# Kernel optimization log

Hardware: AMD Instinct MI355X
Metric: run time of the kernel (lower is better)

Reference implementation:

```python
import jax, jax.numpy as jnp
import numpy as np

BIG = 1e10  # penalty for cross-batch pairs in masked knn


def knn_interpolate(x, pos, pos_skip, batch, batch_skip, k):
    # squared pairwise distances [N_skip, N] via ||a||^2 + ||b||^2 - 2 a.b (avoids [Ns,N,3] temp)
    d2 = (jnp.sum(pos_skip**2, -1)[:, None]
          + jnp.sum(pos**2, -1)[None, :]
          - 2.0 * (pos_skip @ pos.T))
    d2 = jnp.maximum(d2, 0.0)
    # mask out neighbors from a different cloud in the batch
    d2 = d2 + jnp.where(batch_skip[:, None] != batch[None, :], BIG, 0.0)
    neg_d2k, idx = jax.lax.top_k(-d2, k)          # k smallest distances
    d2k = -neg_d2k                                # [N_skip, k]
    w = 1.0 / jnp.clip(d2k, 1e-16)                # inverse squared-distance weights (PyG convention)
    xk = x[idx]                                   # gather neighbor features [N_skip, k, C]
    return jnp.sum(w[..., None] * xk, axis=1) / jnp.sum(w, axis=1, keepdims=True)


def setup_inputs() -> dict:
    key = jax.random.key(0)
    ks = jax.random.split(key, 8)
    B, N, Ns, C, Cs, H = 4, 4096, 16384, 256, 128, 512
    x = jax.random.normal(ks[0], (N, C), dtype=jnp.float32)
    pos = jax.random.normal(ks[1], (N, 3), dtype=jnp.float32)
    batch = jnp.repeat(jnp.arange(B, dtype=jnp.int64), N // B)
    x_skip = jax.random.normal(ks[2], (Ns, Cs), dtype=jnp.float32)
    pos_skip = jax.random.normal(ks[3], (Ns, 3), dtype=jnp.float32)
    batch_skip = jnp.repeat(jnp.arange(B, dtype=jnp.int64), Ns // B)
    fan_in1, fan_in2 = C + Cs, H
    W1 = jax.random.normal(ks[4], (fan_in1, H), dtype=jnp.float32) / np.sqrt(fan_in1)
    b1 = jnp.zeros((H,), dtype=jnp.float32)
    W2 = jax.random.normal(ks[5], (H, H), dtype=jnp.float32) / np.sqrt(fan_in2)
    b2 = jnp.zeros((H,), dtype=jnp.float32)
    return {"x": x, "pos": pos, "batch": batch, "x_skip": x_skip,
            "pos_skip": pos_skip, "batch_skip": batch_skip,
            "W1": W1, "b1": b1, "W2": W2, "b2": b2, "k": 3}


def reference(x, pos, batch, x_skip, pos_skip, batch_skip, W1, b1, W2, b2, k):
    xi = knn_interpolate(x, pos, pos_skip, batch, batch_skip, k)  # [Ns, C]
    h = jnp.concatenate([xi, x_skip], axis=1)                     # [Ns, C+Cs]
    h = jax.nn.relu(h @ W1 + b1)
    h = jax.nn.relu(h @ W2 + b2)
    return (h, pos_skip, batch_skip)
```

## Files before the change

kernel.cpp:

```cpp
#include <hip/hip_runtime.h>
#include <hip/hip_bf16.h>
#include <float.h>


#define KNN_K 3
#define NBATCH 4

typedef __attribute__((ext_vector_type(8))) __bf16 bf16x8;
typedef __attribute__((ext_vector_type(4))) __bf16 bf16x4;
typedef __attribute__((ext_vector_type(4))) float  f32x4;
typedef unsigned long long ull;

__device__ __forceinline__ void gload_lds16(const void* g, void* l) {
    __builtin_amdgcn_global_load_lds(
        (const __attribute__((address_space(1))) unsigned int*)g,
        (__attribute__((address_space(3))) unsigned int*)l, 16, 0, 0);
}

template<int K>
__device__ __forceinline__ void insK(ull (&key)[K], ull c) {
    if (c < key[K-1]) {
        key[K-1] = c;
#pragma unroll
        for (int p = K-1; p >= 1; --p) {
            if (key[p] < key[p-1]) {
                ull t = key[p-1]; key[p-1] = key[p]; key[p] = t;
            }
        }
    }
}

template<int SPAN, int C, int Cs>
__global__ __launch_bounds__(256) void knn_wprep_fast(
    const float* __restrict__ x, const float* __restrict__ pos,
    const int* __restrict__ batch, const float* __restrict__ x_skip,
    const float* __restrict__ pos_skip, const int* __restrict__ batch_skip,
    __bf16* __restrict__ h0, float* __restrict__ out_tail, int Ns,
    const float* __restrict__ W1, const float* __restrict__ W2,
    __bf16* __restrict__ W1t, __bf16* __restrict__ W2t,
    int K1, int H, int H2, int knnBlocks)
{
    __shared__ float4 pos4[SPAN];
    __shared__ ull    skey[256 * KNN_K];
    __shared__ int    sidx[32][KNN_K];
    __shared__ float  swt [32][KNN_K + 1];
    __shared__ float  Ws[32][33];

    const int t = threadIdx.x;

    if (blockIdx.x >= knnBlocks) {
        int b = blockIdx.x - knnBlocks;
        const float* W; __bf16* Wt; int kt, nt, K, Ncols;
        const int nt1 = H / 32, n1 = (K1 / 32) * nt1;
        if (b < n1) { W = W1; Wt = W1t; K = K1; Ncols = H;  kt = b / nt1; nt = b % nt1; }
        else { b -= n1; const int nt2 = H2 / 32;
               W = W2; Wt = W2t; K = H;  Ncols = H2; kt = b / nt2; nt = b % nt2; }
        const int r = t >> 5, c = t & 31;
#pragma unroll
        for (int i = 0; i < 4; ++i)
            Ws[r + i*8][c] = W[(size_t)(kt*32 + r + i*8) * Ncols + nt*32 + c];
        __syncthreads();
#pragma unroll
        for (int i = 0; i < 4; ++i)
            Wt[(size_t)(nt*32 + r + i*8) * K + kt*32 + c] = (__bf16)Ws[c][r + i*8];
        return;
    }

    const int q0 = blockIdx.x * 32;
    const int bs    = batch_skip[q0];
    const int cbase = bs * SPAN;

    for (int i = t; i < SPAN; i += 256) {
        const int j = cbase + i;
        const float qx = pos[j*3+0], qy = pos[j*3+1], qz = pos[j*3+2];
        float pn2 = qx*qx + qy*qy + qz*qz;
        if (batch[j] != bs) pn2 = 3.0e38f;
        pos4[i] = make_float4(qx, qy, qz, pn2);
    }

    if (t < 96)               out_tail[q0*3 + t] = pos_skip[q0*3 + t];
    else if (t < 128)         out_tail[(size_t)Ns*3 + q0 + (t-96)] =
                                  (float)batch_skip[q0 + (t-96)];
    __syncthreads();

    const int q   = t & 31;
    const int g   = t >> 5;
    const int qq  = q0 + q;
    const float px = pos_skip[qq*3+0], py = pos_skip[qq*3+1], pz = pos_skip[qq*3+2];
    const float ps2 = px*px + py*py + pz*pz;

    ull keyA[KNN_K], keyB[KNN_K];
#pragma unroll
    for (int j = 0; j < KNN_K; ++j) { keyA[j] = ~0ull; keyB[j] = ~0ull; }

    const int chunk = SPAN / 8;
    const int half  = chunk / 2;
    const int c0    = g * chunk;
#pragma unroll 4
    for (int i = 0; i < half; ++i) {
        const int jA = c0 + i, jB = c0 + half + i;
        const float4 pA = pos4[jA];
        const float4 pB = pos4[jB];
        float d2A = (ps2 + pA.w) - 2.0f*(px*pA.x + py*pA.y + pz*pA.z);
        float d2B = (ps2 + pB.w) - 2.0f*(px*pB.x + py*pB.y + pz*pB.z);
        d2A = fmaxf(d2A, 0.0f);
        d2B = fmaxf(d2B, 0.0f);
        insK<KNN_K>(keyA, ((ull)__float_as_uint(d2A) << 32) | (unsigned)(cbase + jA));
        insK<KNN_K>(keyB, ((ull)__float_as_uint(d2B) << 32) | (unsigned)(cbase + jB));
    }
#pragma unroll
    for (int j = 0; j < KNN_K; ++j) insK<KNN_K>(keyA, keyB[j]);

#pragma unroll
    for (int j = 0; j < KNN_K; ++j) skey[t*KNN_K + j] = keyA[j];
    __syncthreads();

    if (t < 32) {
        ull key[KNN_K];
#pragma unroll
        for (int j = 0; j < KNN_K; ++j) key[j] = skey[t*KNN_K + j];
#pragma unroll
        for (int gg = 1; gg < 8; ++gg)
#pragma unroll
            for (int j = 0; j < KNN_K; ++j)
                insK<KNN_K>(key, skey[(t + 32*gg)*KNN_K + j]);
        float wv[KNN_K]; float wsum = 0.0f;
#pragma unroll
        for (int j = 0; j < KNN_K; ++j) {
            const float d2 = __uint_as_float((unsigned)(key[j] >> 32));
            sidx[t][j] = (int)(key[j] & 0xFFFFFFFFull);
            wv[j] = 1.0f / fmaxf(d2, 1e-16f);
            wsum += wv[j];
            swt[t][j] = wv[j];
        }
        swt[t][KNN_K] = 1.0f / wsum;
    }
    __syncthreads();

    {
        const int gq  = t >> 3;
        const int sub = t & 7;
        const int s   = q0 + gq;
        const int i0 = sidx[gq][0], i1 = sidx[gq][1], i2 = sidx[gq][2];
        const float w0 = swt[gq][0], w1 = swt[gq][1], w2 = swt[gq][2];
        const float inv = swt[gq][3];
        __bf16* hrow = h0 + (size_t)s * (C + Cs);
        const float* x0 = &x[(size_t)i0*C];
        const float* x1 = &x[(size_t)i1*C];
        const float* x2 = &x[(size_t)i2*C];

#pragma unroll
        for (int cc = 0; cc < C; cc += 32) {
            const int c = cc + sub*4;
            const float4 v0 = *(const float4*)&x0[c];
            const float4 v1 = *(const float4*)&x1[c];
            const float4 v2 = *(const float4*)&x2[c];
            bf16x4 o;
            o[0] = (__bf16)((w0*v0.x + w1*v1.x + w2*v2.x) * inv);
            o[1] = (__bf16)((w0*v0.y + w1*v1.y + w2*v2.y) * inv);
            o[2] = (__bf16)((w0*v0.z + w1*v1.z + w2*v2.z) * inv);
            o[3] = (__bf16)((w0*v0.w + w1*v1.w + w2*v2.w) * inv);
            *(bf16x4*)&hrow[c] = o;
        }
#pragma unroll
        for (int cc = 0; cc < Cs; cc += 32) {
            const int c = cc + sub*4;
            const float4 v = *(const float4*)&x_skip[(size_t)s*Cs + c];
            bf16x4 o;
            o[0] = (__bf16)v.x; o[1] = (__bf16)v.y;
            o[2] = (__bf16)v.z; o[3] = (__bf16)v.w;
            *(bf16x4*)&hrow[C + c] = o;
        }
    }
}

__global__ __launch_bounds__(512) void knn_concat_kernel(
    const float* __restrict__ x, const float* __restrict__ pos,
    const int* __restrict__ batch, const float* __restrict__ x_skip,
    const float* __restrict__ pos_skip, const int* __restrict__ batch_skip,
    __bf16* __restrict__ h0, float* __restrict__ out_tail,
    int N, int C, int Cs, int Ns)
{
    const int t    = threadIdx.x;
    const int lane = t & 63;
    const int wav  = t >> 6;
    const int q0   = blockIdx.x * 64;
    const int q    = q0 + lane;

    __shared__ float4 pos4[1024];
    __shared__ ull    skey[512 * KNN_K];
    __shared__ int    sidx[64][KNN_K];
    __shared__ float  swt [64][KNN_K + 1];

    const int span  = N / NBATCH;
    const int bs    = batch_skip[q0];
    const int cbase = bs * span;

    for (int i = t; i < span; i += 512) {
        const int j = cbase + i;
        const float qx = pos[j*3+0], qy = pos[j*3+1], qz = pos[j*3+2];
        float pn2 = qx*qx + qy*qy + qz*qz;
        if (batch[j] != bs) pn2 = 3.0e38f;
        pos4[i] = make_float4(qx, qy, qz, pn2);
    }
    if (t < 192)              out_tail[q0*3 + t] = pos_skip[q0*3 + t];
    else if (t < 256)         out_tail[(size_t)Ns*3 + q0 + (t-192)] =
                                  (float)batch_skip[q0 + (t-192)];
    __syncthreads();

    const float px = pos_skip[q*3+0], py = pos_skip[q*3+1], pz = pos_skip[q*3+2];
    const float ps2 = px*px + py*py + pz*pz;

    ull key[KNN_K];
#pragma unroll
    for (int j = 0; j < KNN_K; ++j) key[j] = ~0ull;

    const int chunk = span / 8;
    const int c0    = wav * chunk;
#pragma unroll 4
    for (int i = 0; i < chunk; ++i) {
        const int jj = c0 + i;
        const float4 p = pos4[jj];
        const float dot = px*p.x + py*p.y + pz*p.z;
        float d2 = (ps2 + p.w) - 2.0f*dot;
        d2 = fmaxf(d2, 0.0f);
        insK<KNN_K>(key, ((ull)__float_as_uint(d2) << 32) | (unsigned)(cbase + jj));
    }
#pragma unroll
    for (int j = 0; j < KNN_K; ++j) skey[t*KNN_K + j] = key[j];
    __syncthreads();

    if (t < 64) {
#pragma unroll
        for (int ww = 1; ww < 8; ++ww)
#pragma unroll
            for (int j = 0; j < KNN_K; ++j)
                insK<KNN_K>(key, skey[(t + 64*ww)*KNN_K + j]);
        float wv[KNN_K]; float wsum = 0.0f;
#pragma unroll
        for (int j = 0; j < KNN_K; ++j) {
            const float d2 = __uint_as_float((unsigned)(key[j] >> 32));
            sidx[t][j] = (int)(key[j] & 0xFFFFFFFFull);
            wv[j] = 1.0f / fmaxf(d2, 1e-16f);
            wsum += wv[j];
            swt[t][j] = wv[j];
        }
        swt[t][KNN_K] = 1.0f / wsum;
    }
    __syncthreads();

    {
        const int gq  = t >> 3;
        const int sub = t & 7;
        const int s   = q0 + gq;
        const int i0 = sidx[gq][0], i1 = sidx[gq][1], i2 = sidx[gq][2];
        const float w0 = swt[gq][0], w1 = swt[gq][1], w2 = swt[gq][2];
        const float inv = swt[gq][3];
        __bf16* hrow = h0 + (size_t)s * (C + Cs);

        for (int c = sub*4; c < C; c += 32) {
            const float4 v0 = *(const float4*)&x[(size_t)i0*C + c];
            const float4 v1 = *(const float4*)&x[(size_t)i1*C + c];
            const float4 v2 = *(const float4*)&x[(size_t)i2*C + c];
            bf16x4 o;
            o[0] = (__bf16)((w0*v0.x + w1*v1.x + w2*v2.x) * inv);
            o[1] = (__bf16)((w0*v0.y + w1*v1.y + w2*v2.y) * inv);
            o[2] = (__bf16)((w0*v0.z + w1*v1.z + w2*v2.z) * inv);
            o[3] = (__bf16)((w0*v0.w + w1*v1.w + w2*v2.w) * inv);
            *(bf16x4*)&hrow[c] = o;
        }
        for (int c = sub*4; c < Cs; c += 32) {
            const float4 v = *(const float4*)&x_skip[(size_t)s*Cs + c];
            bf16x4 o;
            o[0] = (__bf16)v.x; o[1] = (__bf16)v.y;
            o[2] = (__bf16)v.z; o[3] = (__bf16)v.w;
            *(bf16x4*)&hrow[C + c] = o;
        }
    }
}

__global__ __launch_bounds__(256) void wprep_kernel(
    const float* __restrict__ W1, const float* __restrict__ W2,
    __bf16* __restrict__ W1t, __bf16* __restrict__ W2t,
    int K1, int H, int H2)
{
    __shared__ float Ws[32][33];
    int b = blockIdx.x;
    const float* W; __bf16* Wt; int kt, nt, K, Ncols;
    const int nt1 = H / 32, n1 = (K1 / 32) * nt1;
    if (b < n1) { W = W1; Wt = W1t; K = K1; Ncols = H;  kt = b / nt1; nt = b % nt1; }
    else { b -= n1; const int nt2 = H2 / 32;
           W = W2; Wt = W2t; K = H;  Ncols = H2; kt = b / nt2; nt = b % nt2; }

    const int t = threadIdx.x;
    const int r = t >> 5, c = t & 31;
#pragma unroll
    for (int i = 0; i < 4; ++i)
        Ws[r + i*8][c] = W[(size_t)(kt*32 + r + i*8) * Ncols + nt*32 + c];
    __syncthreads();
#pragma unroll
    for (int i = 0; i < 4; ++i)
        Wt[(size_t)(nt*32 + r + i*8) * K + kt*32 + c] = (__bf16)Ws[c][r + i*8];
}

template<bool OUT_BF16>
__global__ __launch_bounds__(256) void gemm_mfma(
    const __bf16* __restrict__ A,
    const __bf16* __restrict__ Bt,
    const float* __restrict__ bias,
    void* __restrict__ Cout,
    int M, int N, int K)
{
    const int BK = 64;
    __shared__ __bf16 As[128 * BK];
    __shared__ __bf16 Bs[128 * BK];

    const int t    = threadIdx.x;
    const int wave = t >> 6, lane = t & 63;
    const int row0 = blockIdx.y * 128;
    const int col0 = blockIdx.x * 128;
    const int wr   = (wave >> 1) * 64;
    const int wc   = (wave & 1)  * 64;

    const int lr = lane & 15;
    const int lk = (lane >> 4) * 8;

    f32x4 acc[4][4] = {};

    for (int k0 = 0; k0 < K; k0 += BK) {
#pragma unroll
        for (int i = 0; i < 4; ++i) {
            const int ebase = (i*4 + wave) * 512;
            const int e = ebase + lane*8;
            const int r = e >> 6, c = e & 63;
            gload_lds16(&A[(size_t)(row0 + r)*K + k0 + c], &As[ebase]);
        }
#pragma unroll
        for (int i = 0; i < 4; ++i) {
            const int ebase = (i*4 + wave) * 512;
            const int e = ebase + lane*8;
            const int r = e >> 6, c = e & 63;
            gload_lds16(&Bt[(size_t)(col0 + r)*K + k0 + c], &Bs[ebase]);
        }
        __syncthreads();

#pragma unroll
        for (int kk = 0; kk < BK; kk += 32) {
            bf16x8 a[4], b[4];
#pragma unroll
            for (int m = 0; m < 4; ++m)
                a[m] = *(const bf16x8*)&As[(wr + m*16 + lr)*BK + kk + lk];
#pragma unroll
            for (int n = 0; n < 4; ++n)
                b[n] = *(const bf16x8*)&Bs[(wc + n*16 + lr)*BK + kk + lk];
#pragma unroll
            for (int m = 0; m < 4; ++m)
#pragma unroll
                for (int n = 0; n < 4; ++n)
                    acc[m][n] = __builtin_amdgcn_mfma_f32_16x16x32_bf16(
                        a[m], b[n], acc[m][n], 0, 0, 0);
        }
        __syncthreads();
    }

    const int orow = (lane >> 4) * 4;
#pragma unroll
    for (int m = 0; m < 4; ++m) {
#pragma unroll
        for (int n = 0; n < 4; ++n) {
            const int ccol = col0 + wc + n*16 + lr;
            const float bv = bias[ccol];
#pragma unroll
            for (int j = 0; j < 4; ++j) {
                const int crow = row0 + wr + m*16 + orow + j;
                const float v = fmaxf(acc[m][n][j] + bv, 0.0f);
                if (OUT_BF16) ((__bf16*)Cout)[(size_t)crow*N + ccol] = (__bf16)v;
                else          ((float*)Cout)[(size_t)crow*N + ccol]  = v;
            }
        }
    }
}

extern "C" void kernel_launch(void* const* d_in, const int* in_sizes, int n_in,
                              void* d_out, int out_size, void* d_ws, size_t ws_size,
                              hipStream_t stream)
{
    const float* x          = (const float*)d_in[0];
    const float* pos        = (const float*)d_in[1];
    const int*   batch      = (const int*)  d_in[2];
    const float* x_skip     = (const float*)d_in[3];
    const float* pos_skip   = (const float*)d_in[4];
    const int*   batch_skip = (const int*)  d_in[5];
    const float* W1         = (const float*)d_in[6];
    const float* b1         = (const float*)d_in[7];
    const float* W2         = (const float*)d_in[8];
    const float* b2         = (const float*)d_in[9];

    const int N  = in_sizes[2];
    const int Ns = in_sizes[5];
    const int C  = in_sizes[0] / N;
    const int Cs = in_sizes[3] / Ns;
    const int H  = in_sizes[7];
    const int H2 = in_sizes[9];
    const int K1 = C + Cs;

    __bf16* h0  = (__bf16*)d_ws;
    __bf16* h1  = h0  + (size_t)Ns * K1;
    __bf16* W1t = h1  + (size_t)Ns * H;
    __bf16* W2t = W1t + (size_t)H  * K1;
    float*  out = (float*)d_out;

    const int nblk_w = (K1 / 32) * (H / 32) + (H / 32) * (H2 / 32);

    if (N == 4096 && C == 256 && Cs == 128) {
        const int knnBlocks = Ns / 32;
        knn_wprep_fast<1024, 256, 128><<<knnBlocks + nblk_w, 256, 0, stream>>>(
            x, pos, batch, x_skip, pos_skip, batch_skip, h0,
            out + (size_t)Ns * H2, Ns,
            W1, W2, W1t, W2t, K1, H, H2, knnBlocks);
    } else {
        knn_concat_kernel<<<Ns / 64, 512, 0, stream>>>(
            x, pos, batch, x_skip, pos_skip, batch_skip, h0,
            out + (size_t)Ns * H2, N, C, Cs, Ns);
        wprep_kernel<<<nblk_w, 256, 0, stream>>>(W1, W2, W1t, W2t, K1, H, H2);
    }

    dim3 g1(H  / 128, Ns / 128);
    gemm_mfma<true ><<<g1, 256, 0, stream>>>(h0, W1t, b1, (void*)h1, Ns, H,  K1);

    dim3 g2(H2 / 128, Ns / 128);
    gemm_mfma<false><<<g2, 256, 0, stream>>>(h1, W2t, b2, (void*)out, Ns, H2, H);
}
```

Before: 62.25 us.

## Halve queries per KNN block and split candidates into 16 staggered groups

Each KNN block now handles 16 query points instead of 32. Every query's 1024 candidates are split across 16 thread groups instead of 8, and each thread keeps four independent top-3 lists with a group-rotated start index so different groups hit different LDS banks. The grid has twice as many KNN blocks, and the feature-gather phase uses 16 threads per query. The cost is that each block reloads the per-batch candidate positions into shared memory twice as often, and the final serial merge runs over 16 partial lists per query instead of 8.

```diff
diff --git a/kernel.cpp b/kernel.cpp
--- a/kernel.cpp
+++ b/kernel.cpp
@@ -42,8 +42,8 @@
 {
     __shared__ float4 pos4[SPAN];
     __shared__ ull    skey[256 * KNN_K];
-    __shared__ int    sidx[32][KNN_K];
-    __shared__ float  swt [32][KNN_K + 1];
+    __shared__ int    sidx[16][KNN_K];
+    __shared__ float  swt [16][KNN_K + 1];
     __shared__ float  Ws[32][33];
 
     const int t = threadIdx.x;
@@ -66,7 +66,7 @@
         return;
     }
 
-    const int q0 = blockIdx.x * 32;
+    const int q0 = blockIdx.x * 16;
     const int bs    = batch_skip[q0];
     const int cbase = bs * SPAN;
 
@@ -78,52 +78,64 @@
         pos4[i] = make_float4(qx, qy, qz, pn2);
     }
 
-    if (t < 96)               out_tail[q0*3 + t] = pos_skip[q0*3 + t];
-    else if (t < 128)         out_tail[(size_t)Ns*3 + q0 + (t-96)] =
-                                  (float)batch_skip[q0 + (t-96)];
-    __syncthreads();
-
-    const int q   = t & 31;
-    const int g   = t >> 5;
+    if (t < 48)               out_tail[q0*3 + t] = pos_skip[q0*3 + t];
+    else if (t < 64)          out_tail[(size_t)Ns*3 + q0 + (t-48)] =
+                                  (float)batch_skip[q0 + (t-48)];
+    __syncthreads();
+
+    const int q   = t & 15;
+    const int g   = t >> 4;
     const int qq  = q0 + q;
     const float px = pos_skip[qq*3+0], py = pos_skip[qq*3+1], pz = pos_skip[qq*3+2];
     const float ps2 = px*px + py*py + pz*pz;
 
-    ull keyA[KNN_K], keyB[KNN_K];
-#pragma unroll
-    for (int j = 0; j < KNN_K; ++j) { keyA[j] = ~0ull; keyB[j] = ~0ull; }
-
-    const int chunk = SPAN / 8;
-    const int half  = chunk / 2;
-    const int c0    = g * chunk;
+    ull kA[KNN_K], kB[KNN_K], kC[KNN_K], kD[KNN_K];
+#pragma unroll
+    for (int j = 0; j < KNN_K; ++j) { kA[j]=~0ull; kB[j]=~0ull; kC[j]=~0ull; kD[j]=~0ull; }
+
+    const int base = g * (SPAN / 16);
 #pragma unroll 4
-    for (int i = 0; i < half; ++i) {
-        const int jA = c0 + i, jB = c0 + half + i;
+    for (int i = 0; i < 16; ++i) {
+        const int ii = (i + g) & 15;
+        const int jA = base + ii;
+        const int jB = base + 16 + ii;
+        const int jC = base + 32 + ii;
+        const int jD = base + 48 + ii;
         const float4 pA = pos4[jA];
         const float4 pB = pos4[jB];
+        const float4 pC = pos4[jC];
+        const float4 pD = pos4[jD];
         float d2A = (ps2 + pA.w) - 2.0f*(px*pA.x + py*pA.y + pz*pA.z);
         float d2B = (ps2 + pB.w) - 2.0f*(px*pB.x + py*pB.y + pz*pB.z);
-        d2A = fmaxf(d2A, 0.0f);
-        d2B = fmaxf(d2B, 0.0f);
-        insK<KNN_K>(keyA, ((ull)__float_as_uint(d2A) << 32) | (unsigned)(cbase + jA));
-        insK<KNN_K>(keyB, ((ull)__float_as_uint(d2B) << 32) | (unsigned)(cbase + jB));
-    }
-#pragma unroll
-    for (int j = 0; j < KNN_K; ++j) insK<KNN_K>(keyA, keyB[j]);
-
-#pragma unroll
-    for (int j = 0; j < KNN_K; ++j) skey[t*KNN_K + j] = keyA[j];
-    __syncthreads();
-
-    if (t < 32) {
+        float d2C = (ps2 + pC.w) - 2.0f*(px*pC.x + py*pC.y + pz*pC.z);
+        float d2D = (ps2 + pD.w) - 2.0f*(px*pD.x + py*pD.y + pz*pD.z);
+        d2A = fmaxf(d2A, 0.0f); d2B = fmaxf(d2B, 0.0f);
+        d2C = fmaxf(d2C, 0.0f); d2D = fmaxf(d2D, 0.0f);
+        insK<KNN_K>(kA, ((ull)__float_as_uint(d2A) << 32) | (unsigned)(cbase + jA));
+        insK<KNN_K>(kB, ((ull)__float_as_uint(d2B) << 32) | (unsigned)(cbase + jB));
+        insK<KNN_K>(kC, ((ull)__float_as_uint(d2C) << 32) | (unsigned)(cbase + jC));
+        insK<KNN_K>(kD, ((ull)__float_as_uint(d2D) << 32) | (unsigned)(cbase + jD));
+    }
+#pragma unroll
+    for (int j = 0; j < KNN_K; ++j) insK<KNN_K>(kA, kB[j]);
+#pragma unroll
+    for (int j = 0; j < KNN_K; ++j) insK<KNN_K>(kA, kC[j]);
+#pragma unroll
+    for (int j = 0; j < KNN_K; ++j) insK<KNN_K>(kA, kD[j]);
+
+#pragma unroll
+    for (int j = 0; j < KNN_K; ++j) skey[t*KNN_K + j] = kA[j];
+    __syncthreads();
+
+    if (t < 16) {
         ull key[KNN_K];
 #pragma unroll
         for (int j = 0; j < KNN_K; ++j) key[j] = skey[t*KNN_K + j];
 #pragma unroll
-        for (int gg = 1; gg < 8; ++gg)
+        for (int gg = 1; gg < 16; ++gg)
 #pragma unroll
             for (int j = 0; j < KNN_K; ++j)
-                insK<KNN_K>(key, skey[(t + 32*gg)*KNN_K + j]);
+                insK<KNN_K>(key, skey[(t + 16*gg)*KNN_K + j]);
         float wv[KNN_K]; float wsum = 0.0f;
 #pragma unroll
         for (int j = 0; j < KNN_K; ++j) {
@@ -138,8 +150,8 @@
     __syncthreads();
 
     {
-        const int gq  = t >> 3;
-        const int sub = t & 7;
+        const int gq  = t >> 4;
+        const int sub = t & 15;
         const int s   = q0 + gq;
         const int i0 = sidx[gq][0], i1 = sidx[gq][1], i2 = sidx[gq][2];
         const float w0 = swt[gq][0], w1 = swt[gq][1], w2 = swt[gq][2];
@@ -150,7 +162,7 @@
         const float* x2 = &x[(size_t)i2*C];
 
 #pragma unroll
-        for (int cc = 0; cc < C; cc += 32) {
+        for (int cc = 0; cc < C; cc += 64) {
             const int c = cc + sub*4;
             const float4 v0 = *(const float4*)&x0[c];
             const float4 v1 = *(const float4*)&x1[c];
@@ -163,7 +175,7 @@
             *(bf16x4*)&hrow[c] = o;
         }
 #pragma unroll
-        for (int cc = 0; cc < Cs; cc += 32) {
+        for (int cc = 0; cc < Cs; cc += 64) {
             const int c = cc + sub*4;
             const float4 v = *(const float4*)&x_skip[(size_t)s*Cs + c];
             bf16x4 o;
@@ -305,10 +317,8 @@
 
 template<bool OUT_BF16>
 __global__ __launch_bounds__(256) void gemm_mfma(
-    const __bf16* __restrict__ A,
-    const __bf16* __restrict__ Bt,
-    const float* __restrict__ bias,
-    void* __restrict__ Cout,
+    const __bf16* __restrict__ A, const __bf16* __restrict__ Bt,
+    const float* __restrict__ bias, void* __restrict__ Cout,
     int M, int N, int K)
 {
     const int BK = 64;
@@ -413,7 +423,7 @@
     const int nblk_w = (K1 / 32) * (H / 32) + (H / 32) * (H2 / 32);
 
     if (N == 4096 && C == 256 && Cs == 128) {
-        const int knnBlocks = Ns / 32;
+        const int knnBlocks = Ns / 16;
         knn_wprep_fast<1024, 256, 128><<<knnBlocks + nblk_w, 256, 0, stream>>>(
             x, pos, batch, x_skip, pos_skip, batch_skip, h0,
             out + (size_t)Ns * H2, Ns,
```

After: 58.41 us. 6.2% less time.
